# Kernel tuning notes

Measured on AMD Instinct MI355X. Metric: run time of the kernel, lower is better.

## Reference

```python
import jax, jax.numpy as jnp
import numpy as np

B, T, D, H = 1024, 200, 128, 128


def setup_inputs() -> dict:
    key = jax.random.key(0)
    k1, k2, k3, k4 = jax.random.split(key, 4)
    item_his_eb = jax.random.normal(k1, (B, T, D), dtype=jnp.float32)
    seq_len = jax.random.randint(k2, (B,), 0, T, dtype=jnp.int32)
    # TF GRUCell packs [r, u] gates in one matmul over concat([x, h]).
    W_gate = jax.random.normal(k3, (D + H, 2 * H), dtype=jnp.float32) * (1.0 / np.sqrt(D + H))
    b_gate = jnp.ones((2 * H,), dtype=jnp.float32)  # TF GRUCell bias init = 1.0
    W_cand = jax.random.normal(k4, (D + H, H), dtype=jnp.float32) * (1.0 / np.sqrt(D + H))
    b_cand = jnp.zeros((H,), dtype=jnp.float32)
    return {"item_his_eb": item_his_eb, "seq_len": seq_len,
            "W_gate": W_gate, "b_gate": b_gate,
            "W_cand": W_cand, "b_cand": b_cand}


def reference(item_his_eb, seq_len, W_gate, b_gate, W_cand, b_cand):
    # dynamic_rnn(GRUCell(H)) with sequence_length masking.
    # Outputs are zero and state is held for steps t >= seq_len.
    Bq, Tq, Dq = item_his_eb.shape
    Hq = W_cand.shape[1]
    x_tbd = jnp.transpose(item_his_eb, (1, 0, 2))  # [T, B, D]

    def step(h, inp):
        x_t, t = inp  # x_t: [B, D], t: scalar int
        gates = jax.nn.sigmoid(jnp.concatenate([x_t, h], axis=-1) @ W_gate + b_gate)
        r, u = jnp.split(gates, 2, axis=-1)  # each [B, H]
        c = jnp.tanh(jnp.concatenate([x_t, r * h], axis=-1) @ W_cand + b_cand)
        h_new = u * h + (1.0 - u) * c
        valid = (t < seq_len)[:, None]  # [B, 1]
        h_next = jnp.where(valid, h_new, h)
        y = jnp.where(valid, h_new, jnp.zeros_like(h_new))
        return h_next, y

    h0 = jnp.zeros((Bq, Hq), dtype=item_his_eb.dtype)
    _, ys = jax.lax.scan(step, h0, (x_tbd, jnp.arange(Tq)))
    return jnp.transpose(ys, (1, 0, 2))  # [B, T, H]
```

## Files before the change

kernel.cpp:

```cpp
#include <hip/hip_runtime.h>

#define T_SZ 200
#define H_SZ 128

typedef __attribute__((ext_vector_type(8))) short    bf16x8;
typedef __attribute__((ext_vector_type(4))) float    f32x4;
typedef __attribute__((ext_vector_type(4))) int      i32x4;
typedef __attribute__((ext_vector_type(2))) unsigned u32x2;

__device__ __forceinline__ unsigned short f2bf(float f) {
  unsigned u = __builtin_bit_cast(unsigned, f);
  u += 0x7fffu + ((u >> 16) & 1u);
  return (unsigned short)(u >> 16);
}
__device__ __forceinline__ float sigmoid_fast(float x) {
  float e = __builtin_amdgcn_exp2f(-1.442695041f * x);
  return __builtin_amdgcn_rcpf(1.0f + e);
}
__device__ __forceinline__ float tanh_fast(float x) {
  float e = __builtin_amdgcn_exp2f(2.885390082f * x);
  return 1.0f - 2.0f * __builtin_amdgcn_rcpf(e + 1.0f);
}
__device__ __forceinline__ void ldsbar() {
  __asm__ __volatile__("" ::: "memory");
  __builtin_amdgcn_s_waitcnt(0xc07f);
  __builtin_amdgcn_s_barrier();
  __asm__ __volatile__("" ::: "memory");
}

__global__ __launch_bounds__(512, 2) void gru_fused(
    const float* __restrict__ X,
    const int*   __restrict__ seq_len,
    const float* __restrict__ Wg,
    const float* __restrict__ bg,
    const float* __restrict__ Wc,
    const float* __restrict__ bc,
    float* __restrict__ Y)
{
  __shared__ unsigned short hA[16 * 136];
  __shared__ unsigned short rhA[16 * 136];
  __shared__ unsigned short xA[2][16 * 136];
  __shared__ float hT[128 * 20];
  __shared__ float ubuf[128 * 20];

  const int tid  = threadIdx.x;
  const int lane = tid & 63;
  const int w    = tid >> 6;
  const int m16  = lane & 15;
  const int q    = lane >> 4;

  bf16x8 wgf[2][8];
  float  gbias[2];
  #pragma unroll
  for (int nt = 0; nt < 2; ++nt) {
    int col = w * 32 + nt * 16 + m16;
    gbias[nt] = bg[col];
    #pragma unroll
    for (int kb = 0; kb < 8; ++kb) {
      bf16x8 f;
      #pragma unroll
      for (int j = 0; j < 8; ++j)
        f[j] = (short)f2bf(Wg[(size_t)(kb * 32 + q * 8 + j) * 256 + col]);
      wgf[nt][kb] = f;
    }
  }
  const int colc = w * 16 + m16;
  bf16x8 wcf[8];
  float  cbias = bc[colc];
  #pragma unroll
  for (int kb = 0; kb < 8; ++kb) {
    bf16x8 f;
    #pragma unroll
    for (int j = 0; j < 8; ++j)
      f[j] = (short)f2bf(Wc[(size_t)(kb * 32 + q * 8 + j) * 128 + colc]);
    wcf[kb] = f;
  }

  const int bt = blockIdx.x;
  int slen[4];
  #pragma unroll
  for (int i = 0; i < 4; ++i) slen[i] = seq_len[bt * 16 + q * 4 + i];

  float h[4] = {0.f, 0.f, 0.f, 0.f};

  for (int idx = tid; idx < 16 * 136; idx += 512) hA[idx] = 0;
  for (int idx = tid; idx < 128 * 20; idx += 512) hT[idx] = 0.f;

  const int xrow = tid >> 5;
  const int xk4  = (tid & 31) * 4;
  const float* xbase = X + (size_t)(bt * 16 + xrow) * T_SZ * 128 + xk4;

  auto xload = [&](int t, f32x4& r) {
    r = *(const f32x4*)(xbase + (size_t)t * 128);
  };
  auto xstage = [&](int buf, const f32x4& r) {
    unsigned d0 = f2bf(r.x) | ((unsigned)f2bf(r.y) << 16);
    unsigned d1 = f2bf(r.z) | ((unsigned)f2bf(r.w) << 16);
    *(u32x2*)&xA[buf][xrow * 136 + xk4] = (u32x2){d0, d1};
  };

  f32x4 xr0, xr1, xr2, xr3;
  xload(0, xr0);
  xstage(0, xr0);
  xload(1, xr1);
  xload(2, xr2);
  ldsbar();

  float* const ybase = Y + (size_t)(bt * 16 + q * 4) * T_SZ * H_SZ + colc;

  auto step = [&](int t, f32x4& xstage_reg, f32x4& xload_reg) {
    const unsigned short* xb = xA[t & 1];
    bf16x8 xaf[4], haf[4];
    #pragma unroll
    for (int kb = 0; kb < 4; ++kb)
      xaf[kb] = __builtin_bit_cast(bf16x8, *(const i32x4*)&xb[m16 * 136 + kb * 32 + q * 8]);
    #pragma unroll
    for (int kb = 0; kb < 4; ++kb)
      haf[kb] = __builtin_bit_cast(bf16x8, *(const i32x4*)&hA[m16 * 136 + kb * 32 + q * 8]);

    if (t < 199) xstage((t + 1) & 1, xstage_reg);
    if (t < 197) xload(t + 3, xload_reg);

    f32x4 caccx = { cbias, cbias, cbias, cbias };
    #pragma unroll
    for (int kb = 0; kb < 4; ++kb)
      caccx = __builtin_amdgcn_mfma_f32_16x16x32_bf16(xaf[kb], wcf[kb], caccx, 0, 0, 0);

    float racc[2][4];
    #pragma unroll
    for (int nt = 0; nt < 2; ++nt) {
      f32x4 ax = { gbias[nt], gbias[nt], gbias[nt], gbias[nt] };
      #pragma unroll
      for (int kb = 0; kb < 4; ++kb)
        ax = __builtin_amdgcn_mfma_f32_16x16x32_bf16(xaf[kb], wgf[nt][kb], ax, 0, 0, 0);
      f32x4 ah = { 0.f, 0.f, 0.f, 0.f };
      #pragma unroll
      for (int kb = 0; kb < 4; ++kb)
        ah = __builtin_amdgcn_mfma_f32_16x16x32_bf16(haf[kb], wgf[nt][kb + 4], ah, 0, 0, 0);
      #pragma unroll
      for (int i = 0; i < 4; ++i) racc[nt][i] = sigmoid_fast(ax[i] + ah[i]);
    }

    if (w < 4) {
      #pragma unroll
      for (int nt = 0; nt < 2; ++nt) {
        int col = w * 32 + nt * 16 + m16;
        f32x4 hv = *(const f32x4*)&hT[col * 20 + q * 4];
        #pragma unroll
        for (int i = 0; i < 4; ++i)
          rhA[(q * 4 + i) * 136 + col] = f2bf(racc[nt][i] * hv[i]);
      }
    } else {
      #pragma unroll
      for (int nt = 0; nt < 2; ++nt) {
        int colu = (w - 4) * 32 + nt * 16 + m16;
        f32x4 v = { racc[nt][0], racc[nt][1], racc[nt][2], racc[nt][3] };
        *(f32x4*)&ubuf[colu * 20 + q * 4] = v;
      }
    }
    ldsbar();

    bf16x8 rhf[4];
    #pragma unroll
    for (int kb = 0; kb < 4; ++kb)
      rhf[kb] = __builtin_bit_cast(bf16x8, *(const i32x4*)&rhA[m16 * 136 + kb * 32 + q * 8]);
    f32x4 cacc = caccx;
    #pragma unroll
    for (int kb = 0; kb < 4; ++kb)
      cacc = __builtin_amdgcn_mfma_f32_16x16x32_bf16(rhf[kb], wcf[kb + 4], cacc, 0, 0, 0);

    f32x4 uv = *(const f32x4*)&ubuf[colc * 20 + q * 4];
    #pragma unroll
    for (int i = 0; i < 4; ++i) {
      float c  = tanh_fast(cacc[i]);
      float hn = uv[i] * (h[i] - c) + c;
      bool valid = (t < slen[i]);
      float hv = valid ? hn : h[i];
      h[i] = hv;
      ybase[(size_t)i * T_SZ * H_SZ + (size_t)t * H_SZ] = valid ? hn : 0.0f;
      hA[(q * 4 + i) * 136 + colc] = f2bf(hv);
    }
    *(f32x4*)&hT[colc * 20 + q * 4] = (f32x4){ h[0], h[1], h[2], h[3] };
    ldsbar();
  };

  for (int t = 0; t < 200; t += 4) {
    step(t,     xr1, xr3);
    step(t + 1, xr2, xr0);
    step(t + 2, xr3, xr1);
    step(t + 3, xr0, xr2);
  }
}

extern "C" void kernel_launch(void* const* d_in, const int* in_sizes, int n_in,
                              void* d_out, int out_size, void* d_ws, size_t ws_size,
                              hipStream_t stream) {
  const float* X   = (const float*)d_in[0];
  const int*   seq = (const int*)  d_in[1];
  const float* Wg  = (const float*)d_in[2];
  const float* bg  = (const float*)d_in[3];
  const float* Wc  = (const float*)d_in[4];
  const float* bc  = (const float*)d_in[5];
  float* Y = (float*)d_out;
  (void)d_ws; (void)ws_size;

  hipLaunchKernelGGL(gru_fused, dim3(64), dim3(512), 0, stream,
                     X, seq, Wg, bg, Wc, bc, Y);
}
```

Measured before the change: 362.9 us.

## Precompute next step's input projections during current step's recurrent phase

The input-side MFMAs (x·Wg and x·Wc plus biases) for step t+1 now run after the first barrier of step t. They overlap the r*h candidate matmul, so each step's dependent chain holds only the h-side MFMAs. Results pass between steps in ping-pong accumulator registers, with x staged two steps ahead using a reworked load/stage rotation. The h-side MFMA chains are split into two independent accumulators to cut dependency latency. Software bf16 rounding is replaced with v_cvt_pk_bf16_f32, hT loads are hoisted, and launch bounds are relaxed to one block per CU, which trades occupancy for more registers.

```diff
diff --git a/kernel.cpp b/kernel.cpp
--- a/kernel.cpp
+++ b/kernel.cpp
@@ -12,6 +12,11 @@
   unsigned u = __builtin_bit_cast(unsigned, f);
   u += 0x7fffu + ((u >> 16) & 1u);
   return (unsigned short)(u >> 16);
+}
+__device__ __forceinline__ unsigned cvt_pk_bf16(float a, float b) {
+  unsigned r;
+  asm("v_cvt_pk_bf16_f32 %0, %1, %2" : "=v"(r) : "v"(a), "v"(b));
+  return r;
 }
 __device__ __forceinline__ float sigmoid_fast(float x) {
   float e = __builtin_amdgcn_exp2f(-1.442695041f * x);
@@ -28,7 +33,7 @@
   __asm__ __volatile__("" ::: "memory");
 }
 
-__global__ __launch_bounds__(512, 2) void gru_fused(
+__global__ __launch_bounds__(512, 1) void gru_fused(
     const float* __restrict__ X,
     const int*   __restrict__ seq_len,
     const float* __restrict__ Wg,
@@ -94,61 +99,79 @@
     r = *(const f32x4*)(xbase + (size_t)t * 128);
   };
   auto xstage = [&](int buf, const f32x4& r) {
-    unsigned d0 = f2bf(r.x) | ((unsigned)f2bf(r.y) << 16);
-    unsigned d1 = f2bf(r.z) | ((unsigned)f2bf(r.w) << 16);
+    unsigned d0 = cvt_pk_bf16(r.x, r.y);
+    unsigned d1 = cvt_pk_bf16(r.z, r.w);
     *(u32x2*)&xA[buf][xrow * 136 + xk4] = (u32x2){d0, d1};
   };
 
-  f32x4 xr0, xr1, xr2, xr3;
-  xload(0, xr0);
-  xstage(0, xr0);
-  xload(1, xr1);
-  xload(2, xr2);
+  f32x4 x0r, x1r, xrE, xrO;
+  xload(0, x0r); xload(1, x1r);
+  xstage(0, x0r); xstage(1, x1r);
+  xload(2, xrE); xload(3, xrO);
   ldsbar();
 
+  f32x4 axA[2], axB[2], ccA, ccB;
+  {
+    bf16x8 xaf[4];
+    #pragma unroll
+    for (int kb = 0; kb < 4; ++kb)
+      xaf[kb] = __builtin_bit_cast(bf16x8, *(const i32x4*)&xA[0][m16 * 136 + kb * 32 + q * 8]);
+    f32x4 cc = { cbias, cbias, cbias, cbias };
+    #pragma unroll
+    for (int kb = 0; kb < 4; ++kb)
+      cc = __builtin_amdgcn_mfma_f32_16x16x32_bf16(xaf[kb], wcf[kb], cc, 0, 0, 0);
+    ccA = cc;
+    #pragma unroll
+    for (int nt = 0; nt < 2; ++nt) {
+      f32x4 a = { gbias[nt], gbias[nt], gbias[nt], gbias[nt] };
+      #pragma unroll
+      for (int kb = 0; kb < 4; ++kb)
+        a = __builtin_amdgcn_mfma_f32_16x16x32_bf16(xaf[kb], wgf[nt][kb], a, 0, 0, 0);
+      axA[nt] = a;
+    }
+  }
+  ldsbar();
+
   float* const ybase = Y + (size_t)(bt * 16 + q * 4) * T_SZ * H_SZ + colc;
 
-  auto step = [&](int t, f32x4& xstage_reg, f32x4& xload_reg) {
-    const unsigned short* xb = xA[t & 1];
-    bf16x8 xaf[4], haf[4];
-    #pragma unroll
-    for (int kb = 0; kb < 4; ++kb)
-      xaf[kb] = __builtin_bit_cast(bf16x8, *(const i32x4*)&xb[m16 * 136 + kb * 32 + q * 8]);
+  auto step = [&](int t, f32x4& xreg, f32x4* axin, f32x4& ccin,
+                  f32x4* axout, f32x4& ccout) {
+    bf16x8 haf[4];
     #pragma unroll
     for (int kb = 0; kb < 4; ++kb)
       haf[kb] = __builtin_bit_cast(bf16x8, *(const i32x4*)&hA[m16 * 136 + kb * 32 + q * 8]);
-
-    if (t < 199) xstage((t + 1) & 1, xstage_reg);
-    if (t < 197) xload(t + 3, xload_reg);
-
-    f32x4 caccx = { cbias, cbias, cbias, cbias };
-    #pragma unroll
-    for (int kb = 0; kb < 4; ++kb)
-      caccx = __builtin_amdgcn_mfma_f32_16x16x32_bf16(xaf[kb], wcf[kb], caccx, 0, 0, 0);
+    f32x4 hv0, hv1;
+    if (w < 4) {
+      hv0 = *(const f32x4*)&hT[(w * 32 + m16) * 20 + q * 4];
+      hv1 = *(const f32x4*)&hT[(w * 32 + 16 + m16) * 20 + q * 4];
+    }
+    if (t < 198) xstage(t & 1, xreg);
+    if (t < 196) xload(t + 4, xreg);
 
     float racc[2][4];
     #pragma unroll
     for (int nt = 0; nt < 2; ++nt) {
-      f32x4 ax = { gbias[nt], gbias[nt], gbias[nt], gbias[nt] };
-      #pragma unroll
-      for (int kb = 0; kb < 4; ++kb)
-        ax = __builtin_amdgcn_mfma_f32_16x16x32_bf16(xaf[kb], wgf[nt][kb], ax, 0, 0, 0);
-      f32x4 ah = { 0.f, 0.f, 0.f, 0.f };
-      #pragma unroll
-      for (int kb = 0; kb < 4; ++kb)
-        ah = __builtin_amdgcn_mfma_f32_16x16x32_bf16(haf[kb], wgf[nt][kb + 4], ah, 0, 0, 0);
-      #pragma unroll
-      for (int i = 0; i < 4; ++i) racc[nt][i] = sigmoid_fast(ax[i] + ah[i]);
+      f32x4 a = { 0.f, 0.f, 0.f, 0.f }, b = { 0.f, 0.f, 0.f, 0.f };
+      a = __builtin_amdgcn_mfma_f32_16x16x32_bf16(haf[0], wgf[nt][4], a, 0, 0, 0);
+      a = __builtin_amdgcn_mfma_f32_16x16x32_bf16(haf[1], wgf[nt][5], a, 0, 0, 0);
+      b = __builtin_amdgcn_mfma_f32_16x16x32_bf16(haf[2], wgf[nt][6], b, 0, 0, 0);
+      b = __builtin_amdgcn_mfma_f32_16x16x32_bf16(haf[3], wgf[nt][7], b, 0, 0, 0);
+      #pragma unroll
+      for (int i = 0; i < 4; ++i)
+        racc[nt][i] = sigmoid_fast(axin[nt][i] + a[i] + b[i]);
     }
 
     if (w < 4) {
       #pragma unroll
       for (int nt = 0; nt < 2; ++nt) {
+        const f32x4 hv = nt ? hv1 : hv0;
+        unsigned p01 = cvt_pk_bf16(racc[nt][0] * hv.x, racc[nt][1] * hv.y);
+        unsigned p23 = cvt_pk_bf16(racc[nt][2] * hv.z, racc[nt][3] * hv.w);
         int col = w * 32 + nt * 16 + m16;
-        f32x4 hv = *(const f32x4*)&hT[col * 20 + q * 4];
-        #pragma unroll
-        for (int i = 0; i < 4; ++i)
-          rhA[(q * 4 + i) * 136 + col] = f2bf(racc[nt][i] * hv[i]);
+        rhA[(q * 4 + 0) * 136 + col] = (unsigned short)(p01 & 0xffffu);
+        rhA[(q * 4 + 1) * 136 + col] = (unsigned short)(p01 >> 16);
+        rhA[(q * 4 + 2) * 136 + col] = (unsigned short)(p23 & 0xffffu);
+        rhA[(q * 4 + 3) * 136 + col] = (unsigned short)(p23 >> 16);
       }
     } else {
       #pragma unroll
@@ -160,35 +183,63 @@
     }
     ldsbar();
 
+    bf16x8 xaf2[4];
+    if (t < 199) {
+      const unsigned short* xb = xA[(t + 1) & 1];
+      #pragma unroll
+      for (int kb = 0; kb < 4; ++kb)
+        xaf2[kb] = __builtin_bit_cast(bf16x8, *(const i32x4*)&xb[m16 * 136 + kb * 32 + q * 8]);
+    }
     bf16x8 rhf[4];
     #pragma unroll
     for (int kb = 0; kb < 4; ++kb)
       rhf[kb] = __builtin_bit_cast(bf16x8, *(const i32x4*)&rhA[m16 * 136 + kb * 32 + q * 8]);
-    f32x4 cacc = caccx;
-    #pragma unroll
-    for (int kb = 0; kb < 4; ++kb)
-      cacc = __builtin_amdgcn_mfma_f32_16x16x32_bf16(rhf[kb], wcf[kb + 4], cacc, 0, 0, 0);
-
     f32x4 uv = *(const f32x4*)&ubuf[colc * 20 + q * 4];
+
+    if (t < 199) {
+      f32x4 cc = { cbias, cbias, cbias, cbias };
+      #pragma unroll
+      for (int kb = 0; kb < 4; ++kb)
+        cc = __builtin_amdgcn_mfma_f32_16x16x32_bf16(xaf2[kb], wcf[kb], cc, 0, 0, 0);
+      ccout = cc;
+      #pragma unroll
+      for (int nt = 0; nt < 2; ++nt) {
+        f32x4 a = { gbias[nt], gbias[nt], gbias[nt], gbias[nt] };
+        #pragma unroll
+        for (int kb = 0; kb < 4; ++kb)
+          a = __builtin_amdgcn_mfma_f32_16x16x32_bf16(xaf2[kb], wgf[nt][kb], a, 0, 0, 0);
+        axout[nt] = a;
+      }
+    }
+
+    f32x4 ca = { 0.f, 0.f, 0.f, 0.f }, cb = { 0.f, 0.f, 0.f, 0.f };
+    ca = __builtin_amdgcn_mfma_f32_16x16x32_bf16(rhf[0], wcf[4], ca, 0, 0, 0);
+    ca = __builtin_amdgcn_mfma_f32_16x16x32_bf16(rhf[1], wcf[5], ca, 0, 0, 0);
+    cb = __builtin_amdgcn_mfma_f32_16x16x32_bf16(rhf[2], wcf[6], cb, 0, 0, 0);
+    cb = __builtin_amdgcn_mfma_f32_16x16x32_bf16(rhf[3], wcf[7], cb, 0, 0, 0);
+
     #pragma unroll
     for (int i = 0; i < 4; ++i) {
-      float c  = tanh_fast(cacc[i]);
+      float c  = tanh_fast(ccin[i] + ca[i] + cb[i]);
       float hn = uv[i] * (h[i] - c) + c;
       bool valid = (t < slen[i]);
-      float hv = valid ? hn : h[i];
-      h[i] = hv;
+      float hvz = valid ? hn : h[i];
+      h[i] = hvz;
       ybase[(size_t)i * T_SZ * H_SZ + (size_t)t * H_SZ] = valid ? hn : 0.0f;
-      hA[(q * 4 + i) * 136 + colc] = f2bf(hv);
-    }
+    }
+    unsigned hp01 = cvt_pk_bf16(h[0], h[1]);
+    unsigned hp23 = cvt_pk_bf16(h[2], h[3]);
+    hA[(q * 4 + 0) * 136 + colc] = (unsigned short)(hp01 & 0xffffu);
+    hA[(q * 4 + 1) * 136 + colc] = (unsigned short)(hp01 >> 16);
+    hA[(q * 4 + 2) * 136 + colc] = (unsigned short)(hp23 & 0xffffu);
+    hA[(q * 4 + 3) * 136 + colc] = (unsigned short)(hp23 >> 16);
     *(f32x4*)&hT[colc * 20 + q * 4] = (f32x4){ h[0], h[1], h[2], h[3] };
     ldsbar();
   };
 
-  for (int t = 0; t < 200; t += 4) {
-    step(t,     xr1, xr3);
-    step(t + 1, xr2, xr0);
-    step(t + 2, xr3, xr1);
-    step(t + 3, xr0, xr2);
+  for (int t = 0; t < 200; t += 2) {
+    step(t,     xrE, axA, ccA, axB, ccB);
+    step(t + 1, xrO, axB, ccB, axA, ccA);
   }
 }
 
```

Result: no change. 361.0 us (-0.5%).
